# Kernel tuning notes

Measured on AMD Instinct MI355X. Metric: run time of the kernel, lower is better.

The kernel has to match this reference:

```python
import jax, jax.numpy as jnp
import numpy as np

PRECISION = 127.0  # number of discrete pulse-width levels per unit weight


def pwb_quantize(w):
    """PWBMapper: constrain weight to [-1, 1] and snap to `precision` levels."""
    return jnp.round(jnp.clip(w, -1.0, 1.0) * PRECISION) / PRECISION


def setup_inputs() -> dict:
    key = jax.random.key(0)
    kx, kw, kb = jax.random.split(key, 3)
    B, D_in, D_out = 32768, 1024, 128
    x = jax.random.normal(kx, (B, D_in), dtype=jnp.float32)
    # random_normal_initializer default stddev is small; scale a bit but keep in clip range
    W = jax.random.normal(kw, (D_in, D_out), dtype=jnp.float32) * 0.05
    b = jax.random.normal(kb, (D_out,), dtype=jnp.float32) * 0.05
    return {"x": x, "W": W, "b": b}


def reference(x, W, b):
    # Each neuron n.step(data) = dot(quantized weight column, data);
    # bias_neuron.step(e_i) = quantized bias[i].  Activation is identity (None).
    Wq = pwb_quantize(W)          # [D_in, D_out]
    bq = pwb_quantize(b)          # [D_out]
    return x @ Wq + bq            # [B, D_out]
```

## Files before the change

kernel.cpp:

```cpp
#include <hip/hip_runtime.h>
#include <hip/hip_bf16.h>
#include <cstdint>

#define K_DIM 1024
#define N_DIM 128
#define BM 64
#define BK 32
#define NT 32

typedef __attribute__((ext_vector_type(8))) short bf16x8;
typedef __attribute__((ext_vector_type(4))) short bf16x4;
typedef __attribute__((ext_vector_type(4))) float f32x4;
typedef unsigned short u16;
typedef unsigned int u32;

__device__ __forceinline__ float pwbq(float w) {
  w = fminf(fmaxf(w, -1.0f), 1.0f);
  return rintf(w * 127.0f) * (1.0f / 127.0f);
}

__device__ __forceinline__ u16 f2bf(float f) {
  union { float f; u32 u; } v; v.f = f;
  u32 r = v.u + 0x7FFFu + ((v.u >> 16) & 1u);
  return (u16)(r >> 16);
}

__global__ __launch_bounds__(256) void quantW_kernel(const float* __restrict__ W,
                                                     u16* __restrict__ Wimg) {
  int e = blockIdx.x * 256 + threadIdx.x;
  int k = e >> 7;
  int col = e & 127;
  int t = k >> 5, kq = (k >> 3) & 3, j = k & 7;
  Wimg[t * 4096 + (kq * 128 + col) * 8 + j] = f2bf(pwbq(W[e]));
}

__global__ __launch_bounds__(256) void naive_kernel(const float* __restrict__ x,
                                                    const float* __restrict__ W,
                                                    const float* __restrict__ b,
                                                    float* __restrict__ out, int total) {
  int idx = blockIdx.x * 256 + threadIdx.x;
  if (idx >= total) return;
  int m = idx >> 7, n = idx & 127;
  float acc = pwbq(b[n]);
  for (int k = 0; k < K_DIM; ++k)
    acc = fmaf(x[(size_t)m * K_DIM + k], pwbq(W[k * N_DIM + n]), acc);
  out[idx] = acc;
}

__global__ __launch_bounds__(512, 4) void pwb_gemm(
    const float* __restrict__ x,
    const u16* __restrict__ Wimg,
    const float* __restrict__ bias,
    float* __restrict__ out) {

  __shared__ __align__(16) u16 Al[3][BM * BK];
  __shared__ __align__(16) u16 Bl[3][N_DIM * BK];

  const int tid  = threadIdx.x;
  const int lane = tid & 63;
  const int wid  = tid >> 6;
  const int wr   = wid >> 2;
  const int wc   = wid & 3;
  const int m0   = blockIdx.x * BM;
  const int l15  = lane & 15;
  const int lg   = lane >> 4;

  const int grow = tid >> 3;
  const int q8   = tid & 7;
  const float* asrc = x + (size_t)(m0 + grow) * K_DIM + q8 * 4;
  const int aoff = ((q8 >> 1) * 64 + grow) * 8 + (q8 & 1) * 4;

  f32x4 areg[3];

#define LOADA(G) do { areg[(G) % 3] = *(const f32x4*)(asrc + (G) * BK); } while (0)

#define WRITEA(G)                                                        \
  do {                                                                   \
    f32x4 r = areg[(G) % 3];                                             \
    union { bf16x4 v; __hip_bfloat162 p[2]; } pa;                        \
    pa.p[0] = __float22bfloat162_rn(make_float2(r[0], r[1]));            \
    pa.p[1] = __float22bfloat162_rn(make_float2(r[2], r[3]));            \
    *(bf16x4*)(&Al[(G) % 3][aoff]) = pa.v;                               \
  } while (0)

#define ISSUEB(T)                                                        \
  do {                                                                   \
    const u16* srcB = Wimg + (size_t)(T) * 4096 + tid * 8;               \
    __builtin_amdgcn_global_load_lds(                                    \
        (const __attribute__((address_space(1))) void*)srcB,             \
        (__attribute__((address_space(3))) void*)(&Bl[(T) % 3][tid * 8]),\
        16, 0, 0);                                                       \
  } while (0)

  f32x4 acc[2][2] = {};

  LOADA(0);
  LOADA(1);
  ISSUEB(0);
  LOADA(2);
  ISSUEB(1);
  asm volatile("s_waitcnt vmcnt(4)" ::: "memory");
  WRITEA(0);

#pragma unroll
  for (int t = 0; t < NT; ++t) {
    if (t <= NT - 3)      asm volatile("s_waitcnt vmcnt(2)" ::: "memory");
    else if (t == NT - 2) asm volatile("s_waitcnt vmcnt(1)" ::: "memory");
    else                  asm volatile("s_waitcnt vmcnt(0)" ::: "memory");

    if (t + 1 < NT) {
      WRITEA(t + 1);
      asm volatile("s_waitcnt lgkmcnt(0)" ::: "memory");
    }
    __builtin_amdgcn_sched_barrier(0);
    asm volatile("s_barrier" ::: "memory");

    if (t + 3 < NT) LOADA(t + 3);
    if (t + 2 < NT) ISSUEB(t + 2);

    const u16* Ab = &Al[t % 3][0];
    const u16* Bb = &Bl[t % 3][0];
    bf16x8 a[2], b[2];
#pragma unroll
    for (int q = 0; q < 2; ++q)
      a[q] = *(const bf16x8*)(Ab + (lg * 64 + wr * 32 + q * 16 + l15) * 8);
#pragma unroll
    for (int f = 0; f < 2; ++f)
      b[f] = *(const bf16x8*)(Bb + (lg * 128 + wc * 32 + f * 16 + l15) * 8);
#pragma unroll
    for (int q = 0; q < 2; ++q)
#pragma unroll
      for (int f = 0; f < 2; ++f)
        acc[q][f] = __builtin_amdgcn_mfma_f32_16x16x32_bf16(a[q], b[f], acc[q][f], 0, 0, 0);
  }
#undef LOADA
#undef WRITEA
#undef ISSUEB

#pragma unroll
  for (int q = 0; q < 2; ++q) {
    const int gr0 = m0 + wr * 32 + q * 16 + lg * 4;
#pragma unroll
    for (int f = 0; f < 2; ++f) {
      const int gc = wc * 32 + f * 16 + l15;
      const float bq = pwbq(bias[gc]);
#pragma unroll
      for (int j = 0; j < 4; ++j)
        out[(size_t)(gr0 + j) * N_DIM + gc] = acc[q][f][j] + bq;
    }
  }
}

extern "C" void kernel_launch(void* const* d_in, const int* in_sizes, int n_in,
                              void* d_out, int out_size, void* d_ws, size_t ws_size,
                              hipStream_t stream) {
  const float* x = (const float*)d_in[0];
  const float* W = (const float*)d_in[1];
  const float* b = (const float*)d_in[2];
  float* out = (float*)d_out;

  const int M = in_sizes[0] / K_DIM;
  const int grid = M / BM;

  const size_t need = (size_t)K_DIM * N_DIM * sizeof(u16);
  if (d_ws != nullptr && ws_size >= need) {
    u16* Wimg = (u16*)d_ws;
    quantW_kernel<<<(K_DIM * N_DIM) / 256, 256, 0, stream>>>(W, Wimg);
    pwb_gemm<<<grid, 512, 0, stream>>>(x, Wimg, b, out);
  } else {
    int total = M * N_DIM;
    naive_kernel<<<(total + 255) / 256, 256, 0, stream>>>(x, W, b, out, total);
  }
}
```

Baseline: 32.41 us.

## Load quantized weight fragments straight from global into registers, bypassing LDS

The pre-quantized weight image is re-laid out so each output column holds 32 contiguous k-values per K-tile. Each wave now loads its own B MFMA fragments directly into registers, double-buffered one tile ahead. This replaces the LDS staging, LDS reads and the B LDS buffers, which cuts shared-memory traffic and footprint. The cost is that waves sharing a column block fetch the same weights redundantly from L2, and global-load latency for B now sits on the critical path. The vmcnt wait counts are adjusted to match the new load order.

```diff
diff --git a/kernel.cpp b/kernel.cpp
--- a/kernel.cpp
+++ b/kernel.cpp
@@ -30,8 +30,7 @@
   int e = blockIdx.x * 256 + threadIdx.x;
   int k = e >> 7;
   int col = e & 127;
-  int t = k >> 5, kq = (k >> 3) & 3, j = k & 7;
-  Wimg[t * 4096 + (kq * 128 + col) * 8 + j] = f2bf(pwbq(W[e]));
+  Wimg[(k >> 5) * 4096 + col * 32 + (k & 31)] = f2bf(pwbq(W[e]));
 }
 
 __global__ __launch_bounds__(256) void naive_kernel(const float* __restrict__ x,
@@ -54,7 +53,6 @@
     float* __restrict__ out) {
 
   __shared__ __align__(16) u16 Al[3][BM * BK];
-  __shared__ __align__(16) u16 Bl[3][N_DIM * BK];
 
   const int tid  = threadIdx.x;
   const int lane = tid & 63;
@@ -83,30 +81,27 @@
     *(bf16x4*)(&Al[(G) % 3][aoff]) = pa.v;                               \
   } while (0)
 
-#define ISSUEB(T)                                                        \
+  const u16* wb = Wimg + (wc * 32 + l15) * 32 + lg * 8;
+  bf16x8 bs[2][2];
+#define LOADB(T)                                                         \
   do {                                                                   \
-    const u16* srcB = Wimg + (size_t)(T) * 4096 + tid * 8;               \
-    __builtin_amdgcn_global_load_lds(                                    \
-        (const __attribute__((address_space(1))) void*)srcB,             \
-        (__attribute__((address_space(3))) void*)(&Bl[(T) % 3][tid * 8]),\
-        16, 0, 0);                                                       \
+    bs[(T) & 1][0] = *(const bf16x8*)(wb + (size_t)(T) * 4096);          \
+    bs[(T) & 1][1] = *(const bf16x8*)(wb + (size_t)(T) * 4096 + 512);    \
   } while (0)
 
   f32x4 acc[2][2] = {};
 
   LOADA(0);
   LOADA(1);
-  ISSUEB(0);
+  LOADB(0);
   LOADA(2);
-  ISSUEB(1);
   asm volatile("s_waitcnt vmcnt(4)" ::: "memory");
   WRITEA(0);
 
 #pragma unroll
   for (int t = 0; t < NT; ++t) {
-    if (t <= NT - 3)      asm volatile("s_waitcnt vmcnt(2)" ::: "memory");
-    else if (t == NT - 2) asm volatile("s_waitcnt vmcnt(1)" ::: "memory");
-    else                  asm volatile("s_waitcnt vmcnt(0)" ::: "memory");
+    if (t <= NT - 3) asm volatile("s_waitcnt vmcnt(1)" ::: "memory");
+    else             asm volatile("s_waitcnt vmcnt(0)" ::: "memory");
 
     if (t + 1 < NT) {
       WRITEA(t + 1);
@@ -115,27 +110,23 @@
     __builtin_amdgcn_sched_barrier(0);
     asm volatile("s_barrier" ::: "memory");
 
+    if (t + 1 < NT) LOADB(t + 1);
     if (t + 3 < NT) LOADA(t + 3);
-    if (t + 2 < NT) ISSUEB(t + 2);
 
     const u16* Ab = &Al[t % 3][0];
-    const u16* Bb = &Bl[t % 3][0];
-    bf16x8 a[2], b[2];
+    bf16x8 a[2];
 #pragma unroll
     for (int q = 0; q < 2; ++q)
       a[q] = *(const bf16x8*)(Ab + (lg * 64 + wr * 32 + q * 16 + l15) * 8);
 #pragma unroll
-    for (int f = 0; f < 2; ++f)
-      b[f] = *(const bf16x8*)(Bb + (lg * 128 + wc * 32 + f * 16 + l15) * 8);
-#pragma unroll
     for (int q = 0; q < 2; ++q)
 #pragma unroll
       for (int f = 0; f < 2; ++f)
-        acc[q][f] = __builtin_amdgcn_mfma_f32_16x16x32_bf16(a[q], b[f], acc[q][f], 0, 0, 0);
+        acc[q][f] = __builtin_amdgcn_mfma_f32_16x16x32_bf16(a[q], bs[t & 1][f], acc[q][f], 0, 0, 0);
   }
 #undef LOADA
 #undef WRITEA
-#undef ISSUEB
+#undef LOADB
 
 #pragma unroll
   for (int q = 0; q < 2; ++q) {
```

Result: slower. 34.49 us (+6.4%).

## Process two K-tiles per barrier with deeper A/B prefetch buffers

Applied to the files above, without the earlier changes.

Unrolls the GEMM main loop so each barrier covers two BK=32 K-steps, which halves the number of block barriers. A staging grows to 4 LDS/register slots and B to 6 LDS slots, so global loads for x and the quantized W are issued further ahead. Total LDS per block rises to about 64KB, which can reduce how many blocks fit on a CU compared with the previous 3-slot layout. That lowers the occupancy available to hide memory latency in this x-streaming, bandwidth-heavy kernel.

```diff
diff --git a/kernel.cpp b/kernel.cpp
--- a/kernel.cpp
+++ b/kernel.cpp
@@ -7,6 +7,7 @@
 #define BM 64
 #define BK 32
 #define NT 32
+#define NR 16
 
 typedef __attribute__((ext_vector_type(8))) short bf16x8;
 typedef __attribute__((ext_vector_type(4))) short bf16x4;
@@ -53,8 +54,8 @@
     const float* __restrict__ bias,
     float* __restrict__ out) {
 
-  __shared__ __align__(16) u16 Al[3][BM * BK];
-  __shared__ __align__(16) u16 Bl[3][N_DIM * BK];
+  __shared__ __align__(16) u16 Al[4][BM * BK];
+  __shared__ __align__(16) u16 Bl[6][N_DIM * BK];
 
   const int tid  = threadIdx.x;
   const int lane = tid & 63;
@@ -70,17 +71,17 @@
   const float* asrc = x + (size_t)(m0 + grow) * K_DIM + q8 * 4;
   const int aoff = ((q8 >> 1) * 64 + grow) * 8 + (q8 & 1) * 4;
 
-  f32x4 areg[3];
+  f32x4 areg[4];
 
-#define LOADA(G) do { areg[(G) % 3] = *(const f32x4*)(asrc + (G) * BK); } while (0)
+#define LOADA(G) do { areg[(G) % 4] = *(const f32x4*)(asrc + (G) * BK); } while (0)
 
 #define WRITEA(G)                                                        \
   do {                                                                   \
-    f32x4 r = areg[(G) % 3];                                             \
+    f32x4 r_ = areg[(G) % 4];                                            \
     union { bf16x4 v; __hip_bfloat162 p[2]; } pa;                        \
-    pa.p[0] = __float22bfloat162_rn(make_float2(r[0], r[1]));            \
-    pa.p[1] = __float22bfloat162_rn(make_float2(r[2], r[3]));            \
-    *(bf16x4*)(&Al[(G) % 3][aoff]) = pa.v;                               \
+    pa.p[0] = __float22bfloat162_rn(make_float2(r_[0], r_[1]));          \
+    pa.p[1] = __float22bfloat162_rn(make_float2(r_[2], r_[3]));          \
+    *(bf16x4*)(&Al[(G) % 4][aoff]) = pa.v;                               \
   } while (0)
 
 #define ISSUEB(T)                                                        \
@@ -88,7 +89,7 @@
     const u16* srcB = Wimg + (size_t)(T) * 4096 + tid * 8;               \
     __builtin_amdgcn_global_load_lds(                                    \
         (const __attribute__((address_space(1))) void*)srcB,             \
-        (__attribute__((address_space(3))) void*)(&Bl[(T) % 3][tid * 8]),\
+        (__attribute__((address_space(3))) void*)(&Bl[(T) % 6][tid * 8]),\
         16, 0, 0);                                                       \
   } while (0)
 
@@ -96,42 +97,62 @@
 
   LOADA(0);
   LOADA(1);
+  __builtin_amdgcn_sched_barrier(0);
+  asm volatile("s_waitcnt vmcnt(0)" ::: "memory");
+  WRITEA(0);
+  WRITEA(1);
+  __builtin_amdgcn_sched_barrier(0);
+  LOADA(2);
+  LOADA(3);
   ISSUEB(0);
-  LOADA(2);
   ISSUEB(1);
-  asm volatile("s_waitcnt vmcnt(4)" ::: "memory");
-  WRITEA(0);
+  __builtin_amdgcn_sched_barrier(0);
+  LOADA(4);
+  LOADA(5);
+  ISSUEB(2);
+  ISSUEB(3);
 
 #pragma unroll
-  for (int t = 0; t < NT; ++t) {
-    if (t <= NT - 3)      asm volatile("s_waitcnt vmcnt(2)" ::: "memory");
-    else if (t == NT - 2) asm volatile("s_waitcnt vmcnt(1)" ::: "memory");
-    else                  asm volatile("s_waitcnt vmcnt(0)" ::: "memory");
+  for (int r = 0; r < NR; ++r) {
+    if (r <= 13)      asm volatile("s_waitcnt vmcnt(4)" ::: "memory");
+    else if (r == 14) asm volatile("s_waitcnt vmcnt(2)" ::: "memory");
+    else              asm volatile("s_waitcnt vmcnt(0)" ::: "memory");
 
-    if (t + 1 < NT) {
-      WRITEA(t + 1);
-      asm volatile("s_waitcnt lgkmcnt(0)" ::: "memory");
-    }
+    asm volatile("s_waitcnt lgkmcnt(0)" ::: "memory");
     __builtin_amdgcn_sched_barrier(0);
     asm volatile("s_barrier" ::: "memory");
 
-    if (t + 3 < NT) LOADA(t + 3);
-    if (t + 2 < NT) ISSUEB(t + 2);
+    if (2 * r + 2 < NT) {
+      WRITEA(2 * r + 2);
+      WRITEA(2 * r + 3);
+    }
+    if (2 * r + 6 < NT) {
+      LOADA(2 * r + 6);
+      LOADA(2 * r + 7);
+    }
+    if (2 * r + 4 < NT) {
+      ISSUEB(2 * r + 4);
+      ISSUEB(2 * r + 5);
+    }
 
-    const u16* Ab = &Al[t % 3][0];
-    const u16* Bb = &Bl[t % 3][0];
-    bf16x8 a[2], b[2];
 #pragma unroll
-    for (int q = 0; q < 2; ++q)
-      a[q] = *(const bf16x8*)(Ab + (lg * 64 + wr * 32 + q * 16 + l15) * 8);
+    for (int u = 0; u < 2; ++u) {
+      const int tt = 2 * r + u;
+      const u16* Ab = &Al[tt % 4][0];
+      const u16* Bb = &Bl[tt % 6][0];
+      bf16x8 a[2], b[2];
 #pragma unroll
-    for (int f = 0; f < 2; ++f)
-      b[f] = *(const bf16x8*)(Bb + (lg * 128 + wc * 32 + f * 16 + l15) * 8);
-#pragma unroll
-    for (int q = 0; q < 2; ++q)
+      for (int q = 0; q < 2; ++q)
+        a[q] = *(const bf16x8*)(Ab + (lg * 64 + wr * 32 + q * 16 + l15) * 8);
 #pragma unroll
       for (int f = 0; f < 2; ++f)
-        acc[q][f] = __builtin_amdgcn_mfma_f32_16x16x32_bf16(a[q], b[f], acc[q][f], 0, 0, 0);
+        b[f] = *(const bf16x8*)(Bb + (lg * 128 + wc * 32 + f * 16 + l15) * 8);
+#pragma unroll
+      for (int q = 0; q < 2; ++q)
+#pragma unroll
+        for (int f = 0; f < 2; ++f)
+          acc[q][f] = __builtin_amdgcn_mfma_f32_16x16x32_bf16(a[q], b[f], acc[q][f], 0, 0, 0);
+    }
   }
 #undef LOADA
 #undef WRITEA
```

New measurement: 33.18 us. +2.4%, slower.
